# Performance work log

Measured on AMD Instinct MI355X. Metric: run time of the kernel, lower is better.

## Reference

```python
import jax, jax.numpy as jnp
import numpy as np

D_K = 64

def setup_inputs() -> dict:
    key = jax.random.key(0)
    ks = jax.random.split(key, 8)
    B, C, H, W = 4, 256, 40, 40
    d_k, d_g, n_rel = 64, 64, 16
    s = lambda fan_in: 1.0 / np.sqrt(fan_in)
    return {
        "x":  jax.random.normal(ks[0], (B, C, H, W), jnp.float32),
        "Wq": jax.random.normal(ks[1], (C, d_k), jnp.float32) * s(C),
        "bq": jnp.zeros((d_k,), jnp.float32),
        "Wk": jax.random.normal(ks[2], (C, d_k), jnp.float32) * s(C),
        "bk": jnp.zeros((d_k,), jnp.float32),
        "Wv": jax.random.normal(ks[3], (C, C), jnp.float32) * s(C),
        "bv": jnp.zeros((C,), jnp.float32),
        "Wg1": jax.random.normal(ks[4], (4, d_g), jnp.float32) * s(4),
        "bg1": jnp.zeros((d_g,), jnp.float32),
        "Wg2": jax.random.normal(ks[5], (d_g, d_g), jnp.float32) * s(d_g),
        "bg2": jnp.zeros((d_g,), jnp.float32),
        "Wgr": jax.random.normal(ks[6], (d_g, n_rel), jnp.float32) * s(d_g),
        "bgr": jnp.zeros((n_rel,), jnp.float32),
    }

def reference(x, Wq, bq, Wk, bk, Wv, bv, Wg1, bg1, Wg2, bg2, Wgr, bgr):
    B, C, H, W = x.shape
    N = H * W
    # [B, N, C] feature tokens
    feats = jnp.transpose(x, (0, 2, 3, 1)).reshape(B, N, C)
    # pseudo-bboxes: (x, y, 1, 1) per pixel
    yy, xx = jnp.meshgrid(jnp.arange(H), jnp.arange(W), indexing="ij")
    bboxes = jnp.stack(
        [xx.astype(jnp.float32), yy.astype(jnp.float32),
         jnp.ones((H, W), jnp.float32), jnp.ones((H, W), jnp.float32)],
        axis=-1).reshape(N, 4)
    # pairwise geometric features [N, N, 4]: diff[m, n] = bboxes[n] - bboxes[m]
    diff = bboxes[None, :, :] - bboxes[:, None, :]
    geo = jnp.log(jnp.abs(diff) + 1e-8)
    # geo embedding MLP -> relation weights
    e = jax.nn.relu(geo @ Wg1 + bg1)            # [N, N, d_g]
    e = jax.nn.relu(e @ Wg2 + bg2)              # [N, N, d_g]
    w_g = jax.nn.relu(e @ Wgr + bgr)            # [N, N, n_rel]
    w_g_mean = w_g.mean(axis=2)                 # [N, N]
    # appearance attention
    q = feats @ Wq + bq                         # [B, N, d_k]
    k = feats @ Wk + bk                         # [B, N, d_k]
    w_a = jax.nn.softmax(jnp.einsum("bnd,bmd->bnm", q, k) / jnp.sqrt(jnp.float32(D_K)), axis=2)
    w_mn = w_a * w_g_mean[None]                 # [B, N, N]
    v = feats @ Wv + bv                         # [B, N, C]
    rel = jnp.einsum("bnm,bmc->bnc", w_mn, v)
    aug = feats + rel
    return jnp.transpose(aug.reshape(B, H, W, C), (0, 3, 1, 2))
```

## Files before the change

### kernel.cpp

```cpp
#include <hip/hip_runtime.h>
#include <hip/hip_bf16.h>
#include <math.h>

#define NTOK 1600
#define CDIM 256
#define DK   64

typedef __attribute__((ext_vector_type(8))) short bf16x8;
typedef __attribute__((ext_vector_type(4))) float f32x4;

__device__ inline unsigned short f2bf(float v) {
    unsigned int u = __float_as_uint(v);
    unsigned int r = (u + 0x7fffu + ((u >> 16) & 1u)) >> 16;
    return (unsigned short)r;
}

__global__ __launch_bounds__(256) void geo_table_kernel(
    const float* __restrict__ W1, const float* __restrict__ b1,
    const float* __restrict__ W2, const float* __restrict__ b2,
    const float* __restrict__ Wgr, const float* __restrict__ bgr,
    float* __restrict__ table)
{
    __shared__ float e1s[4][64];
    __shared__ float e2s[4][64];
    int t = threadIdx.x;
    int w = t >> 6, j = t & 63;
    int idx = blockIdx.x * 4 + w;
    int ady = idx / 40, adx = idx % 40;
    float g0 = logf((float)adx + 1e-8f);
    float g1 = logf((float)ady + 1e-8f);
    float gc = logf(1e-8f);

    float e1 = fmaxf(g0*W1[j] + g1*W1[64+j] + gc*(W1[128+j]+W1[192+j]) + b1[j], 0.f);
    e1s[w][j] = e1;
    __syncthreads();

    float e2 = b2[j];
    #pragma unroll 8
    for (int i = 0; i < 64; ++i) e2 += e1s[w][i] * W2[i*64 + j];
    e2 = fmaxf(e2, 0.f);
    e2s[w][j] = e2;
    __syncthreads();

    int r = j & 15, q = j >> 4;
    float v = (q == 0) ? bgr[r] : 0.f;
    #pragma unroll
    for (int i = 0; i < 16; ++i) v += e2s[w][q*16 + i] * Wgr[(q*16 + i)*16 + r];
    v += __shfl_xor(v, 16); v += __shfl_xor(v, 32);
    v = fmaxf(v, 0.f);
    v += __shfl_xor(v, 1); v += __shfl_xor(v, 2);
    v += __shfl_xor(v, 4); v += __shfl_xor(v, 8);
    if (j == 0) table[idx] = v * (1.f / 16.f);
}

__global__ __launch_bounds__(512) void qkv_kernel(
    const float* __restrict__ x,
    const float* __restrict__ Wq, const float* __restrict__ bq,
    const float* __restrict__ Wk, const float* __restrict__ bk,
    const float* __restrict__ Wv, const float* __restrict__ bv,
    unsigned short* __restrict__ Qb, unsigned short* __restrict__ Kb,
    unsigned short* __restrict__ Vt)
{
    const int N = NTOK;
    int bx = blockIdx.x, jt = blockIdx.y, b = blockIdx.z;
    const float* Wm; const float* bias; int jb, stride;
    if (jt == 0)      { Wm = Wq; bias = bq; jb = 0;         stride = 64;  }
    else if (jt == 1) { Wm = Wk; bias = bk; jb = 0;         stride = 64;  }
    else              { Wm = Wv; bias = bv; jb = (jt-2)*64; stride = 256; }

    __shared__ __align__(16) unsigned short As[64*72];
    __shared__ __align__(16) unsigned short Bs[64*72];

    int t = threadIdx.x;
    int w = t >> 6, l = t & 63;
    int l15 = l & 15, l4 = l >> 4;
    int panel = w >> 1;
    int jhalf = w & 1;
    int n0 = bx * 64;

    f32x4 acc[2];
    acc[0] = (f32x4){0.f,0.f,0.f,0.f};
    acc[1] = (f32x4){0.f,0.f,0.f,0.f};

    for (int kc = 0; kc < 4; ++kc) {
        int k0 = kc * 64;
        __syncthreads();
        #pragma unroll
        for (int p = 0; p < 2; ++p) {
            int idx = p*512 + t;
            int k = idx >> 4, n4 = (idx & 15) * 4;
            float4 xv = *(const float4*)&x[((size_t)(b*CDIM) + k0 + k)*N + n0 + n4];
            As[(n4+0)*72 + k] = f2bf(xv.x); As[(n4+1)*72 + k] = f2bf(xv.y);
            As[(n4+2)*72 + k] = f2bf(xv.z); As[(n4+3)*72 + k] = f2bf(xv.w);
            float4 wv = *(const float4*)&Wm[(size_t)(k0 + k)*stride + jb + n4];
            Bs[(n4+0)*72 + k] = f2bf(wv.x); Bs[(n4+1)*72 + k] = f2bf(wv.y);
            Bs[(n4+2)*72 + k] = f2bf(wv.z); Bs[(n4+3)*72 + k] = f2bf(wv.w);
        }
        __syncthreads();
        #pragma unroll
        for (int ks = 0; ks < 2; ++ks) {
            bf16x8 a = *(const bf16x8*)&As[(panel*16 + l15)*72 + ks*32 + l4*8];
            #pragma unroll
            for (int jj = 0; jj < 2; ++jj) {
                bf16x8 bf = *(const bf16x8*)&Bs[(jhalf*32 + jj*16 + l15)*72 + ks*32 + l4*8];
                acc[jj] = __builtin_amdgcn_mfma_f32_16x16x32_bf16(a, bf, acc[jj], 0, 0, 0);
            }
        }
    }

    if (jt <= 1) {
        unsigned short* outb = (jt == 0 ? Qb : Kb) + (size_t)b*N*DK;
        float scale = (jt == 0) ? 0.125f : 1.0f;
        #pragma unroll
        for (int jj = 0; jj < 2; ++jj) {
            int j = jhalf*32 + jj*16 + l15;
            float bb = bias[j];
            #pragma unroll
            for (int r = 0; r < 4; ++r) {
                int n = n0 + panel*16 + l4*4 + r;
                outb[(size_t)n*DK + j] = f2bf((acc[jj][r] + bb) * scale);
            }
        }
    } else {
        __syncthreads();
        unsigned short* sv = As;
        #pragma unroll
        for (int jj = 0; jj < 2; ++jj) {
            int j = jhalf*32 + jj*16 + l15;
            float bb = bias[jb + j];
            #pragma unroll
            for (int r = 0; r < 4; ++r)
                sv[j*72 + panel*16 + l4*4 + r] = f2bf(acc[jj][r] + bb);
        }
        __syncthreads();
        int c   = t >> 3;
        int off = (t & 7) * 8;
        uint4 v = *(const uint4*)&sv[c*72 + off];
        *(uint4*)&Vt[((size_t)b*CDIM + jb + c)*N + n0 + off] = v;
    }
}

__global__ __launch_bounds__(256) void attn_kernel(
    const float* __restrict__ x, const float* __restrict__ gtab,
    const unsigned short* __restrict__ Qb, const unsigned short* __restrict__ Kb,
    const unsigned short* __restrict__ Vt, float* __restrict__ out)
{
    const int N = NTOK, C = CDIM;
    int b = blockIdx.z, c0 = blockIdx.y * 64, n0 = blockIdx.x * 16;
    int t = threadIdx.x;
    int w = t >> 6, l = t & 63;
    int l15 = l & 15, l4 = l >> 4;

    __shared__ __align__(16) unsigned short Pl[2][16*72];
    __shared__ float sh_g[NTOK];
    __shared__ float shZ[4][16];
    __shared__ float zsum[16];
    __shared__ __align__(16) float outs[64*17];

    for (int p = t; p < NTOK; p += 256) sh_g[p] = gtab[p];

    const unsigned short* qrow = &Qb[((size_t)b*N + n0 + l15)*DK + l4*8];
    bf16x8 qa0 = *(const bf16x8*)qrow;
    bf16x8 qa1 = *(const bf16x8*)(qrow + 32);

    f32x4 acc = (f32x4){0.f,0.f,0.f,0.f};
    float z[4] = {0.f, 0.f, 0.f, 0.f};

    int yn[4], xn[4];
    #pragma unroll
    for (int r = 0; r < 4; ++r) {
        int n = n0 + l4*4 + r;
        yn[r] = n / 40; xn[r] = n - 40*yn[r];
    }
    int mcol = w*16 + l15;

    __syncthreads();

    for (int cc = 0; cc < 25; ++cc) {
        int m0 = cc * 64;
        int mg = m0 + mcol;
        const unsigned short* kbase = &Kb[((size_t)b*N + mg)*DK + l4*8];
        bf16x8 kb0 = *(const bf16x8*)kbase;
        bf16x8 kb1 = *(const bf16x8*)(kbase + 32);
        f32x4 s4 = (f32x4){0.f,0.f,0.f,0.f};
        s4 = __builtin_amdgcn_mfma_f32_16x16x32_bf16(qa0, kb0, s4, 0, 0, 0);
        s4 = __builtin_amdgcn_mfma_f32_16x16x32_bf16(qa1, kb1, s4, 0, 0, 0);

        int ym = mg / 40, xm = mg - 40*ym;
        unsigned short* prow = &Pl[cc & 1][0];
        #pragma unroll
        for (int r = 0; r < 4; ++r) {
            float e = __expf(s4[r]);
            z[r] += e;
            int ady = ym - yn[r]; ady = ady < 0 ? -ady : ady;
            int adx = xm - xn[r]; adx = adx < 0 ? -adx : adx;
            prow[(l4*4 + r)*72 + mcol] = f2bf(e * sh_g[ady*40 + adx]);
        }
        __syncthreads();

        const unsigned short* pb = &Pl[cc & 1][l15*72 + l4*8];
        bf16x8 pa0 = *(const bf16x8*)pb;
        bf16x8 pa1 = *(const bf16x8*)(pb + 32);
        const unsigned short* vb = &Vt[((size_t)b*C + c0 + w*16 + l15)*N + m0 + l4*8];
        bf16x8 v0 = *(const bf16x8*)vb;
        bf16x8 v1 = *(const bf16x8*)(vb + 32);
        acc = __builtin_amdgcn_mfma_f32_16x16x32_bf16(pa0, v0, acc, 0, 0, 0);
        acc = __builtin_amdgcn_mfma_f32_16x16x32_bf16(pa1, v1, acc, 0, 0, 0);
    }

    #pragma unroll
    for (int r = 0; r < 4; ++r) {
        float v = z[r];
        v += __shfl_xor(v, 1); v += __shfl_xor(v, 2);
        v += __shfl_xor(v, 4); v += __shfl_xor(v, 8);
        if (l15 == 0) shZ[w][l4*4 + r] = v;
    }
    #pragma unroll
    for (int r = 0; r < 4; ++r)
        outs[(w*16 + l15)*17 + l4*4 + r] = acc[r];
    __syncthreads();

    if (t < 16) zsum[t] = 1.f / (shZ[0][t] + shZ[1][t] + shZ[2][t] + shZ[3][t]);
    __syncthreads();

    int c  = t >> 2;
    int nl = (t & 3) * 4;
    size_t gi = ((size_t)b*C + c0 + c)*N + n0 + nl;
    float4 xv = *(const float4*)&x[gi];
    float4 o;
    o.x = xv.x + outs[c*17 + nl + 0] * zsum[nl + 0];
    o.y = xv.y + outs[c*17 + nl + 1] * zsum[nl + 1];
    o.z = xv.z + outs[c*17 + nl + 2] * zsum[nl + 2];
    o.w = xv.w + outs[c*17 + nl + 3] * zsum[nl + 3];
    *(float4*)&out[gi] = o;
}

extern "C" void kernel_launch(void* const* d_in, const int* in_sizes, int n_in,
                              void* d_out, int out_size, void* d_ws, size_t ws_size,
                              hipStream_t stream)
{
    const float* x   = (const float*)d_in[0];
    const float* Wq  = (const float*)d_in[1];
    const float* bq  = (const float*)d_in[2];
    const float* Wk  = (const float*)d_in[3];
    const float* bk  = (const float*)d_in[4];
    const float* Wv  = (const float*)d_in[5];
    const float* bv  = (const float*)d_in[6];
    const float* Wg1 = (const float*)d_in[7];
    const float* bg1 = (const float*)d_in[8];
    const float* Wg2 = (const float*)d_in[9];
    const float* bg2 = (const float*)d_in[10];
    const float* Wgr = (const float*)d_in[11];
    const float* bgr = (const float*)d_in[12];

    char* ws = (char*)d_ws;
    float* table       = (float*)ws;
    unsigned short* Qb = (unsigned short*)(ws + 8192);
    unsigned short* Kb = (unsigned short*)(ws + 8192 + 819200);
    unsigned short* Vt = (unsigned short*)(ws + 8192 + 2*819200);

    geo_table_kernel<<<dim3(400), dim3(256), 0, stream>>>(Wg1, bg1, Wg2, bg2, Wgr, bgr, table);
    qkv_kernel<<<dim3(25, 6, 4), dim3(512), 0, stream>>>(x, Wq, bq, Wk, bk, Wv, bv, Qb, Kb, Vt);
    attn_kernel<<<dim3(100, 4, 4), dim3(256), 0, stream>>>(x, table, Qb, Kb, Vt, (float*)d_out);
}
```

Baseline: 184.6 us.

## Prefetch next K/V and QKV input tiles into registers, use LDS-only barriers

The QKV projection loop now loads the next 64-wide K chunk of x or the weights into registers while the current chunk is converted and written to shared memory. Half the threads load x and half load weights, using strided scalar loads. The attention loop prefetches the next tile's K and V fragments into registers before computing the current tile. Block barriers are replaced with a wait on LDS counters plus s_barrier, so outstanding global loads can keep running across the barrier. The cost is more live registers, which may lower occupancy, and narrower scalar loads in the projection.

```diff
diff --git a/kernel.cpp b/kernel.cpp
--- a/kernel.cpp
+++ b/kernel.cpp
@@ -13,6 +13,12 @@
     unsigned int u = __float_as_uint(v);
     unsigned int r = (u + 0x7fffu + ((u >> 16) & 1u)) >> 16;
     return (unsigned short)r;
+}
+
+__device__ inline void lgkm_barrier() {
+    asm volatile("s_waitcnt lgkmcnt(0)" ::: "memory");
+    __builtin_amdgcn_s_barrier();
+    asm volatile("" ::: "memory");
 }
 
 __global__ __launch_bounds__(256) void geo_table_kernel(
@@ -78,25 +84,44 @@
     int jhalf = w & 1;
     int n0 = bx * 64;
 
+    int g  = t & 63;
+    int kq = (t & 255) >> 6;
+    bool isA = (t < 256);
+
+    float rcur[16], rnxt[16];
+
+    #define QKV_LOAD(k0g, dst)                                                   \
+        if (isA) {                                                               \
+            const float* base_ = &x[((size_t)(b*CDIM) + (k0g) + kq*16)*N + n0 + g]; \
+            _Pragma("unroll")                                                    \
+            for (int kk = 0; kk < 16; ++kk) (dst)[kk] = base_[(size_t)kk*N];     \
+        } else {                                                                 \
+            const float* base_ = &Wm[(size_t)((k0g) + kq*16)*stride + jb + g];   \
+            _Pragma("unroll")                                                    \
+            for (int kk = 0; kk < 16; ++kk) (dst)[kk] = base_[(size_t)kk*stride];\
+        }
+
+    QKV_LOAD(0, rcur);
+
     f32x4 acc[2];
     acc[0] = (f32x4){0.f,0.f,0.f,0.f};
     acc[1] = (f32x4){0.f,0.f,0.f,0.f};
 
+    unsigned short* dstT = isA ? As : Bs;
+
+    #pragma unroll
     for (int kc = 0; kc < 4; ++kc) {
-        int k0 = kc * 64;
-        __syncthreads();
-        #pragma unroll
-        for (int p = 0; p < 2; ++p) {
-            int idx = p*512 + t;
-            int k = idx >> 4, n4 = (idx & 15) * 4;
-            float4 xv = *(const float4*)&x[((size_t)(b*CDIM) + k0 + k)*N + n0 + n4];
-            As[(n4+0)*72 + k] = f2bf(xv.x); As[(n4+1)*72 + k] = f2bf(xv.y);
-            As[(n4+2)*72 + k] = f2bf(xv.z); As[(n4+3)*72 + k] = f2bf(xv.w);
-            float4 wv = *(const float4*)&Wm[(size_t)(k0 + k)*stride + jb + n4];
-            Bs[(n4+0)*72 + k] = f2bf(wv.x); Bs[(n4+1)*72 + k] = f2bf(wv.y);
-            Bs[(n4+2)*72 + k] = f2bf(wv.z); Bs[(n4+3)*72 + k] = f2bf(wv.w);
-        }
-        __syncthreads();
+        lgkm_barrier();
+        #pragma unroll
+        for (int jq = 0; jq < 4; ++jq) {
+            __align__(8) unsigned short u[4];
+            #pragma unroll
+            for (int i2 = 0; i2 < 4; ++i2) u[i2] = f2bf(rcur[jq*4 + i2]);
+            *(uint2*)&dstT[g*72 + kq*16 + jq*4] = *(const uint2*)u;
+        }
+        QKV_LOAD(kc < 3 ? (kc+1)*64 : 0, rnxt);
+        lgkm_barrier();
+
         #pragma unroll
         for (int ks = 0; ks < 2; ++ks) {
             bf16x8 a = *(const bf16x8*)&As[(panel*16 + l15)*72 + ks*32 + l4*8];
@@ -106,6 +131,8 @@
                 acc[jj] = __builtin_amdgcn_mfma_f32_16x16x32_bf16(a, bf, acc[jj], 0, 0, 0);
             }
         }
+        #pragma unroll
+        for (int i = 0; i < 16; ++i) rcur[i] = rnxt[i];
     }
 
     if (jt <= 1) {
@@ -174,18 +201,31 @@
     }
     int mcol = w*16 + l15;
 
+    const unsigned short* kb_base = &Kb[((size_t)b*N + mcol)*DK + l4*8];
+    const unsigned short* vb_base = &Vt[((size_t)b*C + c0 + w*16 + l15)*N + l4*8];
+
+    bf16x8 kb0 = *(const bf16x8*)(kb_base);
+    bf16x8 kb1 = *(const bf16x8*)(kb_base + 32);
+    bf16x8 vb0 = *(const bf16x8*)(vb_base);
+    bf16x8 vb1 = *(const bf16x8*)(vb_base + 32);
+
     __syncthreads();
 
     for (int cc = 0; cc < 25; ++cc) {
         int m0 = cc * 64;
-        int mg = m0 + mcol;
-        const unsigned short* kbase = &Kb[((size_t)b*N + mg)*DK + l4*8];
-        bf16x8 kb0 = *(const bf16x8*)kbase;
-        bf16x8 kb1 = *(const bf16x8*)(kbase + 32);
+        int mnext = (cc < 24) ? m0 + 64 : 0;
+        const unsigned short* kp = kb_base + (size_t)mnext*64;
+        const unsigned short* vp = vb_base + mnext;
+        bf16x8 kn0 = *(const bf16x8*)(kp);
+        bf16x8 kn1 = *(const bf16x8*)(kp + 32);
+        bf16x8 vn0 = *(const bf16x8*)(vp);
+        bf16x8 vn1 = *(const bf16x8*)(vp + 32);
+
         f32x4 s4 = (f32x4){0.f,0.f,0.f,0.f};
         s4 = __builtin_amdgcn_mfma_f32_16x16x32_bf16(qa0, kb0, s4, 0, 0, 0);
         s4 = __builtin_amdgcn_mfma_f32_16x16x32_bf16(qa1, kb1, s4, 0, 0, 0);
 
+        int mg = m0 + mcol;
         int ym = mg / 40, xm = mg - 40*ym;
         unsigned short* prow = &Pl[cc & 1][0];
         #pragma unroll
@@ -196,16 +236,15 @@
             int adx = xm - xn[r]; adx = adx < 0 ? -adx : adx;
             prow[(l4*4 + r)*72 + mcol] = f2bf(e * sh_g[ady*40 + adx]);
         }
-        __syncthreads();
+        lgkm_barrier();
 
         const unsigned short* pb = &Pl[cc & 1][l15*72 + l4*8];
         bf16x8 pa0 = *(const bf16x8*)pb;
         bf16x8 pa1 = *(const bf16x8*)(pb + 32);
-        const unsigned short* vb = &Vt[((size_t)b*C + c0 + w*16 + l15)*N + m0 + l4*8];
-        bf16x8 v0 = *(const bf16x8*)vb;
-        bf16x8 v1 = *(const bf16x8*)(vb + 32);
-        acc = __builtin_amdgcn_mfma_f32_16x16x32_bf16(pa0, v0, acc, 0, 0, 0);
-        acc = __builtin_amdgcn_mfma_f32_16x16x32_bf16(pa1, v1, acc, 0, 0, 0);
+        acc = __builtin_amdgcn_mfma_f32_16x16x32_bf16(pa0, vb0, acc, 0, 0, 0);
+        acc = __builtin_amdgcn_mfma_f32_16x16x32_bf16(pa1, vb1, acc, 0, 0, 0);
+
+        kb0 = kn0; kb1 = kn1; vb0 = vn0; vb1 = vn1;
     }
 
     #pragma unroll
```

Result: no change. 186.1 us (+0.8%).
